# Kernel optimization log

Measured on AMD Instinct MI355X. Metric: run time of the kernel, lower is better.

Reference implementation:

```python
import jax, jax.numpy as jnp
import numpy as np

REGION_MAX = 116
DEFAULT_REGION_ID = 0


def setup_inputs() -> dict:
    key = jax.random.key(0)
    k1, k2, k3, k4 = jax.random.split(key, 4)
    B, N = 16, 4096
    D, H, W = 182, 218, 182
    embed_dim = 768
    # patch centers in MRI voxel space; range slightly exceeds the atlas so
    # some points land out-of-bounds and exercise the default-region path.
    patch_centers_voxels = jax.random.uniform(k1, (B, N, 3), dtype=jnp.float32) * 230.0 - 20.0
    # use identity-like affines (typical co-registered case)
    mri_affine = jnp.eye(4, dtype=jnp.float32)
    aal_affine = jnp.eye(4, dtype=jnp.float32)
    # atlas volume with integer region labels stored as float (nib get_fdata)
    aal_data = jax.random.randint(k3, (D, H, W), 0, REGION_MAX + 1).astype(jnp.float32)
    embed_table = jax.random.normal(k4, (REGION_MAX + 1, embed_dim), dtype=jnp.float32)
    return {
        "patch_centers_voxels": patch_centers_voxels,
        "mri_affine": mri_affine,
        "aal_affine": aal_affine,
        "aal_data": aal_data,
        "embed_table": embed_table,
    }


def reference(patch_centers_voxels, mri_affine, aal_affine, aal_data, embed_table):
    B, N, _ = patch_centers_voxels.shape
    D, H, W = aal_data.shape
    # homogeneous voxel coords -> world coords -> atlas voxel coords
    ones = jnp.ones((B, N, 1), dtype=patch_centers_voxels.dtype)
    voxel_homo = jnp.concatenate([patch_centers_voxels, ones], axis=-1)  # [B,N,4]
    world = jnp.einsum('ij,bnj->bni', mri_affine, voxel_homo)
    inv_aal = jnp.linalg.inv(aal_affine)
    aal_vox = jnp.einsum('ij,bnj->bni', inv_aal, world)[..., :3]  # [B,N,3]
    idx = jnp.round(aal_vox).astype(jnp.int32)  # [B,N,3]
    x, y, z = idx[..., 0], idx[..., 1], idx[..., 2]
    in_bounds = (
        (x >= 0) & (x < D) & (y >= 0) & (y < H) & (z >= 0) & (z < W)
    )
    cx = jnp.clip(x, 0, D - 1)
    cy = jnp.clip(y, 0, H - 1)
    cz = jnp.clip(z, 0, W - 1)
    region = aal_data[cx, cy, cz].astype(jnp.int32)  # [B,N]
    valid = in_bounds & (region >= 0) & (region <= REGION_MAX)
    region_ids = jnp.where(valid, region, DEFAULT_REGION_ID)
    return embed_table[region_ids]  # [B,N,embed_dim]
```

## Files before the change

### kernel.cpp

```cpp
#include <hip/hip_runtime.h>
#include <math.h>

#define REGION_MAX 116
#define EMB 768
#define DIM_D 182
#define DIM_H 218
#define DIM_W 182

__global__ void compute_M_kernel(const float* __restrict__ mri,
                                 const float* __restrict__ aal,
                                 float* __restrict__ M) {
    if (threadIdx.x != 0 || blockIdx.x != 0) return;
    float a[4][8];
    for (int i = 0; i < 4; ++i)
        for (int j = 0; j < 4; ++j) {
            a[i][j]     = aal[i * 4 + j];
            a[i][j + 4] = (i == j) ? 1.0f : 0.0f;
        }
    for (int c = 0; c < 4; ++c) {
        int piv = c;
        float best = fabsf(a[c][c]);
        for (int r = c + 1; r < 4; ++r) {
            float v = fabsf(a[r][c]);
            if (v > best) { best = v; piv = r; }
        }
        if (piv != c)
            for (int j = 0; j < 8; ++j) {
                float t = a[c][j]; a[c][j] = a[piv][j]; a[piv][j] = t;
            }
        float inv = 1.0f / a[c][c];
        for (int j = 0; j < 8; ++j) a[c][j] *= inv;
        for (int r = 0; r < 4; ++r) {
            if (r == c) continue;
            float f = a[r][c];
            for (int j = 0; j < 8; ++j) a[r][j] -= f * a[c][j];
        }
    }
    for (int i = 0; i < 3; ++i)
        for (int j = 0; j < 4; ++j) {
            float s = 0.0f;
            for (int k = 0; k < 4; ++k) s += a[i][4 + k] * mri[k * 4 + j];
            M[i * 4 + j] = s;
        }
}

__global__ __launch_bounds__(256) void aal_embed_kernel(
    const float* __restrict__ centers,
    const float* __restrict__ M,
    const float* __restrict__ vol,
    const float* __restrict__ table,
    float* __restrict__ out,
    int P) {
    int wave = (blockIdx.x * blockDim.x + threadIdx.x) >> 6;
    int lane = threadIdx.x & 63;
    if (wave >= P) return;

    float px = centers[wave * 3 + 0];
    float py = centers[wave * 3 + 1];
    float pz = centers[wave * 3 + 2];

    float fx = M[0] * px + M[1] * py + M[2]  * pz + M[3];
    float fy = M[4] * px + M[5] * py + M[6]  * pz + M[7];
    float fz = M[8] * px + M[9] * py + M[10] * pz + M[11];

    int x = (int)rintf(fx);
    int y = (int)rintf(fy);
    int z = (int)rintf(fz);

    bool inb = (x >= 0) & (x < DIM_D) & (y >= 0) & (y < DIM_H) &
               (z >= 0) & (z < DIM_W);
    int cx = min(max(x, 0), DIM_D - 1);
    int cy = min(max(y, 0), DIM_H - 1);
    int cz = min(max(z, 0), DIM_W - 1);

    int region = (int)vol[((size_t)cx * DIM_H + cy) * DIM_W + cz];
    int rid = (inb && region >= 0 && region <= REGION_MAX) ? region : 0;

    const float4* __restrict__ src = (const float4*)(table + (size_t)rid * EMB);
    float4* __restrict__ dst = (float4*)(out + (size_t)wave * EMB);
    dst[lane]       = src[lane];
    dst[lane + 64]  = src[lane + 64];
    dst[lane + 128] = src[lane + 128];
}

extern "C" void kernel_launch(void* const* d_in, const int* in_sizes, int n_in,
                              void* d_out, int out_size, void* d_ws, size_t ws_size,
                              hipStream_t stream) {
    const float* centers = (const float*)d_in[0];
    const float* mri     = (const float*)d_in[1];
    const float* aal     = (const float*)d_in[2];
    const float* vol     = (const float*)d_in[3];
    const float* table   = (const float*)d_in[4];
    float* out = (float*)d_out;
    float* M   = (float*)d_ws;

    int P = in_sizes[0] / 3;

    compute_M_kernel<<<1, 64, 0, stream>>>(mri, aal, M);

    int waves_per_block = 256 / 64;
    int blocks = (P + waves_per_block - 1) / waves_per_block;
    aal_embed_kernel<<<blocks, 256, 0, stream>>>(centers, M, vol, table, out, P);
}
```

Measured before the change: 236.7 us.

## Split region lookup and embedding copy into separate kernels with nontemporal stores

Fuses the affine-inverse computation into a per-point region kernel, where each block computes M into shared memory and each thread handles one point, writing region ids to workspace. A second flat kernel copies embedding rows float4 by float4 with nontemporal stores, so every thread does uniform work and the latency of the dependent volume gather is taken off the copy path. The cost is an extra kernel launch, a workspace round trip for the ids, and every block redoing the small 4x4 inverse.

```diff
diff --git a/kernel.cpp b/kernel.cpp
--- a/kernel.cpp
+++ b/kernel.cpp
@@ -3,61 +3,62 @@
 
 #define REGION_MAX 116
 #define EMB 768
+#define EMB4 192
 #define DIM_D 182
 #define DIM_H 218
 #define DIM_W 182
 
-__global__ void compute_M_kernel(const float* __restrict__ mri,
-                                 const float* __restrict__ aal,
-                                 float* __restrict__ M) {
-    if (threadIdx.x != 0 || blockIdx.x != 0) return;
-    float a[4][8];
-    for (int i = 0; i < 4; ++i)
-        for (int j = 0; j < 4; ++j) {
-            a[i][j]     = aal[i * 4 + j];
-            a[i][j + 4] = (i == j) ? 1.0f : 0.0f;
+typedef float v4f __attribute__((ext_vector_type(4)));
+
+__global__ __launch_bounds__(256) void region_kernel(
+    const float* __restrict__ centers,
+    const float* __restrict__ mri,
+    const float* __restrict__ aal,
+    const float* __restrict__ vol,
+    int* __restrict__ rid_out,
+    int P) {
+    __shared__ float M[12];
+    if (threadIdx.x == 0) {
+        float a[4][8];
+        for (int i = 0; i < 4; ++i)
+            for (int j = 0; j < 4; ++j) {
+                a[i][j]     = aal[i * 4 + j];
+                a[i][j + 4] = (i == j) ? 1.0f : 0.0f;
+            }
+        for (int c = 0; c < 4; ++c) {
+            int piv = c;
+            float best = fabsf(a[c][c]);
+            for (int r = c + 1; r < 4; ++r) {
+                float v = fabsf(a[r][c]);
+                if (v > best) { best = v; piv = r; }
+            }
+            if (piv != c)
+                for (int j = 0; j < 8; ++j) {
+                    float t = a[c][j]; a[c][j] = a[piv][j]; a[piv][j] = t;
+                }
+            float inv = 1.0f / a[c][c];
+            for (int j = 0; j < 8; ++j) a[c][j] *= inv;
+            for (int r = 0; r < 4; ++r) {
+                if (r == c) continue;
+                float f = a[r][c];
+                for (int j = 0; j < 8; ++j) a[r][j] -= f * a[c][j];
+            }
         }
-    for (int c = 0; c < 4; ++c) {
-        int piv = c;
-        float best = fabsf(a[c][c]);
-        for (int r = c + 1; r < 4; ++r) {
-            float v = fabsf(a[r][c]);
-            if (v > best) { best = v; piv = r; }
-        }
-        if (piv != c)
-            for (int j = 0; j < 8; ++j) {
-                float t = a[c][j]; a[c][j] = a[piv][j]; a[piv][j] = t;
+        for (int i = 0; i < 3; ++i)
+            for (int j = 0; j < 4; ++j) {
+                float s = 0.0f;
+                for (int k = 0; k < 4; ++k) s += a[i][4 + k] * mri[k * 4 + j];
+                M[i * 4 + j] = s;
             }
-        float inv = 1.0f / a[c][c];
-        for (int j = 0; j < 8; ++j) a[c][j] *= inv;
-        for (int r = 0; r < 4; ++r) {
-            if (r == c) continue;
-            float f = a[r][c];
-            for (int j = 0; j < 8; ++j) a[r][j] -= f * a[c][j];
-        }
     }
-    for (int i = 0; i < 3; ++i)
-        for (int j = 0; j < 4; ++j) {
-            float s = 0.0f;
-            for (int k = 0; k < 4; ++k) s += a[i][4 + k] * mri[k * 4 + j];
-            M[i * 4 + j] = s;
-        }
-}
+    __syncthreads();
 
-__global__ __launch_bounds__(256) void aal_embed_kernel(
-    const float* __restrict__ centers,
-    const float* __restrict__ M,
-    const float* __restrict__ vol,
-    const float* __restrict__ table,
-    float* __restrict__ out,
-    int P) {
-    int wave = (blockIdx.x * blockDim.x + threadIdx.x) >> 6;
-    int lane = threadIdx.x & 63;
-    if (wave >= P) return;
+    int p = blockIdx.x * blockDim.x + threadIdx.x;
+    if (p >= P) return;
 
-    float px = centers[wave * 3 + 0];
-    float py = centers[wave * 3 + 1];
-    float pz = centers[wave * 3 + 2];
+    float px = centers[p * 3 + 0];
+    float py = centers[p * 3 + 1];
+    float pz = centers[p * 3 + 2];
 
     float fx = M[0] * px + M[1] * py + M[2]  * pz + M[3];
     float fy = M[4] * px + M[5] * py + M[6]  * pz + M[7];
@@ -74,13 +75,22 @@
     int cz = min(max(z, 0), DIM_W - 1);
 
     int region = (int)vol[((size_t)cx * DIM_H + cy) * DIM_W + cz];
-    int rid = (inb && region >= 0 && region <= REGION_MAX) ? region : 0;
+    rid_out[p] = (inb && region >= 0 && region <= REGION_MAX) ? region : 0;
+}
 
-    const float4* __restrict__ src = (const float4*)(table + (size_t)rid * EMB);
-    float4* __restrict__ dst = (float4*)(out + (size_t)wave * EMB);
-    dst[lane]       = src[lane];
-    dst[lane + 64]  = src[lane + 64];
-    dst[lane + 128] = src[lane + 128];
+__global__ __launch_bounds__(256) void copy_kernel(
+    const int* __restrict__ rid,
+    const float* __restrict__ table,
+    float* __restrict__ out,
+    long total4) {
+    long i = (long)blockIdx.x * blockDim.x + threadIdx.x;
+    if (i >= total4) return;
+    long p = i / EMB4;
+    int  c = (int)(i - p * EMB4);
+    int  r = rid[p];
+    const v4f* __restrict__ src = (const v4f*)(table) + (long)r * EMB4 + c;
+    v4f v = *src;
+    __builtin_nontemporal_store(v, ((v4f*)out) + i);
 }
 
 extern "C" void kernel_launch(void* const* d_in, const int* in_sizes, int n_in,
@@ -92,13 +102,14 @@
     const float* vol     = (const float*)d_in[3];
     const float* table   = (const float*)d_in[4];
     float* out = (float*)d_out;
-    float* M   = (float*)d_ws;
+    int*   rid = (int*)d_ws;
 
     int P = in_sizes[0] / 3;
 
-    compute_M_kernel<<<1, 64, 0, stream>>>(mri, aal, M);
+    int blocks1 = (P + 255) / 256;
+    region_kernel<<<blocks1, 256, 0, stream>>>(centers, mri, aal, vol, rid, P);
 
-    int waves_per_block = 256 / 64;
-    int blocks = (P + waves_per_block - 1) / waves_per_block;
-    aal_embed_kernel<<<blocks, 256, 0, stream>>>(centers, M, vol, table, out, P);
+    long total4 = (long)P * EMB4;
+    int blocks2 = (int)((total4 + 255) / 256);
+    copy_kernel<<<blocks2, 256, 0, stream>>>(rid, table, out, total4);
 }
```

After: 223.6 us. -5.5%, faster.
